# Performance work log

Measured on AMD Instinct MI355X. Metric: run time of the kernel, lower is better.

Reference implementation:

```python
import jax, jax.numpy as jnp
import numpy as np

N_USER, N_ITEM = 100000, 50000
D, H, B, E = 64, 64, 16384, 2000000

def _xavier(key, shape):
    fan_in, fan_out = shape[0], shape[1]
    lim = float(np.sqrt(6.0 / (fan_in + fan_out)))
    return jax.random.uniform(key, shape, jnp.float32, -lim, lim)

def setup_inputs() -> dict:
    key = jax.random.key(0)
    ks = jax.random.split(key, 16)
    inp = {
        "user_table": _xavier(ks[0], (N_USER, D)),
        "item_table": _xavier(ks[1], (N_ITEM, D)),
        "Wu": _xavier(ks[2], (D, D)),   # GCN_user weight ([in,out])
        "bu": jnp.zeros((D,), jnp.float32),
        "Wi": _xavier(ks[3], (D, D)),   # GCN_item weight
        "bi": jnp.zeros((D,), jnp.float32),
        "W1": _xavier(ks[4], (4 * D, 2 * H)),
        "b1": jnp.zeros((2 * H,), jnp.float32),
        "W2": _xavier(ks[5], (2 * H, H)),
        "b2": jnp.zeros((H,), jnp.float32),
        "W3": _xavier(ks[6], (H, 1)),
        "b3": jnp.zeros((1,), jnp.float32),
        "user_bias": jnp.zeros((N_USER, 1), jnp.float32),
        "item_bias": jnp.zeros((N_ITEM, 1), jnp.float32),
        "user_id": jax.random.randint(ks[7], (B,), 0, N_USER),
        "item_id": jax.random.randint(ks[8], (B,), 0, N_ITEM),
        "edge_user": jax.random.randint(ks[9], (E,), 0, N_USER),
        "edge_item": jax.random.randint(ks[10], (E,), 0, N_ITEM),
    }
    return inp

def reference(user_table, item_table, Wu, bu, Wi, bi, W1, b1, W2, b2, W3, b3,
              user_bias, item_bias, user_id, item_id, edge_user, edge_item):
    # sparse.mm(edge_ui, item_h)[user_id]: aggregate item embeddings per user
    agg_i = jax.ops.segment_sum(item_table[edge_item], edge_user, num_segments=N_USER)[user_id]
    agg_u = jax.ops.segment_sum(user_table[edge_user], edge_item, num_segments=N_ITEM)[item_id]
    ones_e = jnp.ones((edge_user.shape[0],), jnp.float32)
    deg_u = jax.ops.segment_sum(ones_e, edge_user, num_segments=N_USER)[user_id] + 1.0  # item_din
    deg_i = jax.ops.segment_sum(ones_e, edge_item, num_segments=N_ITEM)[item_id] + 1.0  # user_din
    gcn_item_h = agg_i / deg_u[:, None]   # [B, D]
    gcn_user_h = agg_u / deg_i[:, None]   # [B, D]
    # dropout p=0.3 is identity in eval mode
    gcn_user_out = jax.nn.relu(gcn_user_h @ Wu + bu)
    gcn_item_out = jax.nn.relu(gcn_item_h @ Wi + bi)
    u_emb = user_table[user_id]
    i_emb = item_table[item_id]
    x = jnp.concatenate([u_emb * i_emb,
                         u_emb * gcn_item_out,
                         gcn_user_out * i_emb,
                         gcn_user_out * gcn_item_out], axis=-1)  # [B, 4D]
    x1 = jnp.tanh(x @ W1 + b1)
    x2 = jnp.tanh(x1 @ W2 + b2)
    x3 = (x2 @ W3 + b3).reshape(-1)
    return x3 + user_bias[user_id, 0] + item_bias[item_id, 0]
```

## Files before the change

kernel.cpp:

```cpp
#include <hip/hip_runtime.h>
#include <cstdint>
#include <cstddef>

#define D 64
#define CAPU 96
#define CAPI 128
#define OCAP 4096
#define GR 32

__global__ __launch_bounds__(256) void k_build_maps(const int* __restrict__ user_id,
                                                    const int* __restrict__ item_id,
                                                    int* __restrict__ map_u,
                                                    int* __restrict__ map_i, int B)
{
    int i = blockIdx.x * blockDim.x + threadIdx.x;
    if (i < B) {
        atomicCAS(&map_u[user_id[i]], -1, i);
        atomicCAS(&map_i[item_id[i]], -1, i);
    }
}

__global__ __launch_bounds__(256) void k_scatter(const int* __restrict__ edge_user,
                                                 const int* __restrict__ edge_item,
                                                 const int* __restrict__ map_u,
                                                 const int* __restrict__ map_i,
                                                 int* __restrict__ cntU,
                                                 int* __restrict__ cntI,
                                                 uint32_t* __restrict__ listU,
                                                 uint32_t* __restrict__ listI,
                                                 int* __restrict__ ovfCnt,
                                                 uint32_t* __restrict__ ovf, int E)
{
    int t = blockIdx.x * blockDim.x + threadIdx.x;
    int base = t * 2;
    if (base >= E) return;

    int u0, u1 = -1, i0, i1 = 0;
    if (base + 2 <= E) {
        int2 eu = *(const int2*)(edge_user + base);
        int2 ei = *(const int2*)(edge_item + base);
        u0 = eu.x; u1 = eu.y; i0 = ei.x; i1 = ei.y;
    } else {
        u0 = edge_user[base]; i0 = edge_item[base];
    }

    int su0 = map_u[u0];
    int si0 = map_i[i0];
    int su1 = (u1 >= 0) ? map_u[u1] : -1;
    int si1 = (u1 >= 0) ? map_i[i1] : -1;

    if (su0 >= 0) {
        int pos = atomicAdd(&cntU[su0 * 16], 1);
        if (pos < CAPU) listU[(size_t)su0 * CAPU + pos] = (uint32_t)i0;
        else { int o = atomicAdd(ovfCnt, 1);
               if (o < OCAP) ovf[o] = ((uint32_t)su0 << 17) | (uint32_t)i0; }
    }
    if (si0 >= 0) {
        int pos = atomicAdd(&cntI[si0 * 16], 1);
        if (pos < CAPI) listI[(size_t)si0 * CAPI + pos] = (uint32_t)u0;
        else { int o = atomicAdd(ovfCnt, 1);
               if (o < OCAP) ovf[o] = 0x80000000u | ((uint32_t)si0 << 17) | (uint32_t)u0; }
    }
    if (su1 >= 0) {
        int pos = atomicAdd(&cntU[su1 * 16], 1);
        if (pos < CAPU) listU[(size_t)su1 * CAPU + pos] = (uint32_t)i1;
        else { int o = atomicAdd(ovfCnt, 1);
               if (o < OCAP) ovf[o] = ((uint32_t)su1 << 17) | (uint32_t)i1; }
    }
    if (si1 >= 0) {
        int pos = atomicAdd(&cntI[si1 * 16], 1);
        if (pos < CAPI) listI[(size_t)si1 * CAPI + pos] = (uint32_t)u1;
        else { int o = atomicAdd(ovfCnt, 1);
               if (o < OCAP) ovf[o] = 0x80000000u | ((uint32_t)si1 << 17) | (uint32_t)u1; }
    }
}

__global__ __launch_bounds__(256) void k_gather(const uint32_t* __restrict__ listU,
                                                const uint32_t* __restrict__ listI,
                                                const int* __restrict__ cntU,
                                                const int* __restrict__ cntI,
                                                const float* __restrict__ user_table,
                                                const float* __restrict__ item_table,
                                                const int* __restrict__ ovfCnt,
                                                const uint32_t* __restrict__ ovf,
                                                float* __restrict__ aggIU,
                                                float* __restrict__ aggUI, int B)
{
    int gg = (blockIdx.x * blockDim.x + threadIdx.x) >> 4;
    if (gg >= 2 * B) return;
    int l16 = threadIdx.x & 15;
    int side = gg >= B;
    int slot = side ? gg - B : gg;

    int cnt = side ? cntI[slot * 16] : cntU[slot * 16];
    int caps = side ? CAPI : CAPU;
    int n = cnt < caps ? cnt : caps;
    const uint32_t* list = side ? (listI + (size_t)slot * CAPI)
                                : (listU + (size_t)slot * CAPU);
    const float4* table4 = (const float4*)(side ? user_table : item_table);

    float4 a0 = {0.f,0.f,0.f,0.f}, a1 = {0.f,0.f,0.f,0.f};
    float4 a2 = {0.f,0.f,0.f,0.f}, a3 = {0.f,0.f,0.f,0.f};
    int j = 0;
    for (; j + 8 <= n; j += 8) {
        int r0 = (int)list[j],   r1 = (int)list[j+1], r2 = (int)list[j+2], r3 = (int)list[j+3];
        int r4 = (int)list[j+4], r5 = (int)list[j+5], r6 = (int)list[j+6], r7 = (int)list[j+7];
        float4 v0 = table4[(size_t)r0 * 16 + l16];
        float4 v1 = table4[(size_t)r1 * 16 + l16];
        float4 v2 = table4[(size_t)r2 * 16 + l16];
        float4 v3 = table4[(size_t)r3 * 16 + l16];
        float4 v4 = table4[(size_t)r4 * 16 + l16];
        float4 v5 = table4[(size_t)r5 * 16 + l16];
        float4 v6 = table4[(size_t)r6 * 16 + l16];
        float4 v7 = table4[(size_t)r7 * 16 + l16];
        a0.x += v0.x; a0.y += v0.y; a0.z += v0.z; a0.w += v0.w;
        a1.x += v1.x; a1.y += v1.y; a1.z += v1.z; a1.w += v1.w;
        a2.x += v2.x; a2.y += v2.y; a2.z += v2.z; a2.w += v2.w;
        a3.x += v3.x; a3.y += v3.y; a3.z += v3.z; a3.w += v3.w;
        a0.x += v4.x; a0.y += v4.y; a0.z += v4.z; a0.w += v4.w;
        a1.x += v5.x; a1.y += v5.y; a1.z += v5.z; a1.w += v5.w;
        a2.x += v6.x; a2.y += v6.y; a2.z += v6.z; a2.w += v6.w;
        a3.x += v7.x; a3.y += v7.y; a3.z += v7.z; a3.w += v7.w;
    }
    for (; j < n; ++j) {
        int r0 = (int)list[j];
        float4 v0 = table4[(size_t)r0 * 16 + l16];
        a0.x += v0.x; a0.y += v0.y; a0.z += v0.z; a0.w += v0.w;
    }
    if (cnt > caps) {
        int on = *ovfCnt; if (on > OCAP) on = OCAP;
        for (int k = 0; k < on; ++k) {
            uint32_t p = ovf[k];
            if ((int)(p >> 31) == side && (int)((p >> 17) & 0x3FFFu) == slot) {
                float4 v = table4[(size_t)(p & 0x1FFFFu) * 16 + l16];
                a0.x += v.x; a0.y += v.y; a0.z += v.z; a0.w += v.w;
            }
        }
    }
    float inv = 1.0f / ((float)cnt + 1.0f);
    float4 acc = {(a0.x+a1.x+a2.x+a3.x) * inv, (a0.y+a1.y+a2.y+a3.y) * inv,
                  (a0.z+a1.z+a2.z+a3.z) * inv, (a0.w+a1.w+a2.w+a3.w) * inv};
    float4* agg4 = (float4*)(side ? aggUI : aggIU);
    agg4[(size_t)slot * 16 + l16] = acc;
}

__global__ __launch_bounds__(256) void k_gcn_mlp(const int* __restrict__ user_id,
                                                 const int* __restrict__ item_id,
                                                 const int* __restrict__ map_u,
                                                 const int* __restrict__ map_i,
                                                 const float* __restrict__ aggIU,
                                                 const float* __restrict__ aggUI,
                                                 const float* __restrict__ user_table,
                                                 const float* __restrict__ item_table,
                                                 const float* __restrict__ Wi,
                                                 const float* __restrict__ bi,
                                                 const float* __restrict__ Wu,
                                                 const float* __restrict__ bu,
                                                 const float* __restrict__ W1,
                                                 const float* __restrict__ b1,
                                                 const float* __restrict__ W2,
                                                 const float* __restrict__ b2,
                                                 const float* __restrict__ W3,
                                                 const float* __restrict__ b3,
                                                 const float* __restrict__ user_bias,
                                                 const float* __restrict__ item_bias,
                                                 float* __restrict__ out, int B)
{
    __shared__ float XgiL[GR][68];
    __shared__ float XguL[GR][68];
    __shared__ float Fbuf[2 * GR][68];
    __shared__ float WB[8192];
    __shared__ int sU[GR], sI[GR];
    int t = threadIdx.x;
    int row0 = blockIdx.x * GR;
    if (t < GR) { sU[t] = user_id[row0 + t]; sI[t] = item_id[row0 + t]; }
    __syncthreads();

    int txg = t & 15, tyg = t >> 4;
    {
        const float4* agg4 = (const float4*)aggIU;
        #pragma unroll
        for (int q = 0; q < 2; ++q) {
            int idx = t * 2 + q; int r = idx >> 4, l16 = idx & 15;
            int slot = map_u[sU[r]];
            ((float4*)&Fbuf[r][0])[l16] = agg4[(size_t)slot * 16 + l16];
        }
        const float4* wg = (const float4*)Wi;
        float4* d = (float4*)WB;
        #pragma unroll
        for (int q = 0; q < 4; ++q) d[t + q * 256] = wg[t + q * 256];
    }
    __syncthreads();
    {
        float acc[2][4] = {};
        for (int k = 0; k < 64; ++k) {
            float a0 = Fbuf[2 * tyg][k], a1 = Fbuf[2 * tyg + 1][k];
            #pragma unroll
            for (int c = 0; c < 4; ++c) {
                float w = WB[k * 64 + txg + 16 * c];
                acc[0][c] = fmaf(a0, w, acc[0][c]);
                acc[1][c] = fmaf(a1, w, acc[1][c]);
            }
        }
        #pragma unroll
        for (int r = 0; r < 2; ++r)
            #pragma unroll
            for (int c = 0; c < 4; ++c)
                XgiL[2 * tyg + r][txg + 16 * c] = fmaxf(acc[r][c] + bi[txg + 16 * c], 0.f);
    }
    __syncthreads();
    {
        const float4* agg4 = (const float4*)aggUI;
        #pragma unroll
        for (int q = 0; q < 2; ++q) {
            int idx = t * 2 + q; int r = idx >> 4, l16 = idx & 15;
            int slot = map_i[sI[r]];
            ((float4*)&Fbuf[r][0])[l16] = agg4[(size_t)slot * 16 + l16];
        }
        const float4* wg = (const float4*)Wu;
        float4* d = (float4*)WB;
        #pragma unroll
        for (int q = 0; q < 4; ++q) d[t + q * 256] = wg[t + q * 256];
    }
    __syncthreads();
    {
        float acc[2][4] = {};
        for (int k = 0; k < 64; ++k) {
            float a0 = Fbuf[2 * tyg][k], a1 = Fbuf[2 * tyg + 1][k];
            #pragma unroll
            for (int c = 0; c < 4; ++c) {
                float w = WB[k * 64 + txg + 16 * c];
                acc[0][c] = fmaf(a0, w, acc[0][c]);
                acc[1][c] = fmaf(a1, w, acc[1][c]);
            }
        }
        #pragma unroll
        for (int r = 0; r < 2; ++r)
            #pragma unroll
            for (int c = 0; c < 4; ++c)
                XguL[2 * tyg + r][txg + 16 * c] = fmaxf(acc[r][c] + bu[txg + 16 * c], 0.f);
    }
    __syncthreads();

    #pragma unroll
    for (int q = 0; q < 2; ++q) {
        int idx = t * 2 + q; int r = idx >> 4, l16 = idx & 15;
        ((float4*)&Fbuf[r][0])[l16] = ((const float4*)user_table)[(size_t)sU[r] * 16 + l16];
        ((float4*)&Fbuf[GR + r][0])[l16] = ((const float4*)item_table)[(size_t)sI[r] * 16 + l16];
    }

    int tx1 = t & 31, ty1 = t >> 5;
    float acc1[4][4] = {};
    for (int j = 0; j < 4; ++j) {
        {
            const float4* w4 = (const float4*)W1 + (size_t)j * 2048;
            float4* d = (float4*)WB;
            #pragma unroll
            for (int q = 0; q < 8; ++q) d[t + q * 256] = w4[t + q * 256];
        }
        __syncthreads();
        const float (*FA)[68] = (j < 2) ? (const float (*)[68])&Fbuf[0] : (const float (*)[68])XguL;
        const float (*FB)[68] = ((j & 1) == 0) ? (const float (*)[68])&Fbuf[GR] : (const float (*)[68])XgiL;
        for (int k = 0; k < 64; ++k) {
            float a[4], b[4];
            #pragma unroll
            for (int r = 0; r < 4; ++r) a[r] = FA[4 * ty1 + r][k] * FB[4 * ty1 + r][k];
            #pragma unroll
            for (int c = 0; c < 4; ++c) b[c] = WB[k * 128 + tx1 + 32 * c];
            #pragma unroll
            for (int r = 0; r < 4; ++r)
                #pragma unroll
                for (int c = 0; c < 4; ++c)
                    acc1[r][c] = fmaf(a[r], b[c], acc1[r][c]);
        }
        __syncthreads();
    }

    float* x1t = &Fbuf[0][0];
    #pragma unroll
    for (int r = 0; r < 4; ++r)
        #pragma unroll
        for (int c = 0; c < 4; ++c) {
            int col = tx1 + 32 * c;
            x1t[(4 * ty1 + r) * 132 + col] = tanhf(acc1[r][c] + b1[col]);
        }
    {
        const float4* w4 = (const float4*)W2;
        float4* d = (float4*)WB;
        #pragma unroll
        for (int q = 0; q < 8; ++q) d[t + q * 256] = w4[t + q * 256];
    }
    __syncthreads();

    int tx2 = t & 15, ty2 = t >> 4;
    float acc2[2][4] = {};
    for (int k = 0; k < 128; ++k) {
        float a0 = x1t[(2 * ty2) * 132 + k];
        float a1 = x1t[(2 * ty2 + 1) * 132 + k];
        #pragma unroll
        for (int c = 0; c < 4; ++c) {
            float w = WB[k * 64 + tx2 + 16 * c];
            acc2[0][c] = fmaf(a0, w, acc2[0][c]);
            acc2[1][c] = fmaf(a1, w, acc2[1][c]);
        }
    }
    float b3v = b3[0];
    #pragma unroll
    for (int r = 0; r < 2; ++r) {
        int lr = 2 * ty2 + r;
        float p = 0.f;
        #pragma unroll
        for (int c = 0; c < 4; ++c) {
            int col = tx2 + 16 * c;
            p += tanhf(acc2[r][c] + b2[col]) * W3[col];
        }
        p += __shfl_xor(p, 1);
        p += __shfl_xor(p, 2);
        p += __shfl_xor(p, 4);
        p += __shfl_xor(p, 8);
        if (tx2 == 0)
            out[row0 + lr] = p + b3v + user_bias[sU[lr]] + item_bias[sI[lr]];
    }
}

extern "C" void kernel_launch(void* const* d_in, const int* in_sizes, int n_in,
                              void* d_out, int out_size, void* d_ws, size_t ws_size,
                              hipStream_t stream)
{
    const float* user_table = (const float*)d_in[0];
    const float* item_table = (const float*)d_in[1];
    const float* Wu = (const float*)d_in[2];
    const float* bu = (const float*)d_in[3];
    const float* Wi = (const float*)d_in[4];
    const float* bi = (const float*)d_in[5];
    const float* W1 = (const float*)d_in[6];
    const float* b1 = (const float*)d_in[7];
    const float* W2 = (const float*)d_in[8];
    const float* b2 = (const float*)d_in[9];
    const float* W3 = (const float*)d_in[10];
    const float* b3 = (const float*)d_in[11];
    const float* user_bias = (const float*)d_in[12];
    const float* item_bias = (const float*)d_in[13];
    const int* user_id = (const int*)d_in[14];
    const int* item_id = (const int*)d_in[15];
    const int* edge_user = (const int*)d_in[16];
    const int* edge_item = (const int*)d_in[17];

    const int N_USER = in_sizes[0] / D;
    const int N_ITEM = in_sizes[1] / D;
    const int B = in_sizes[14];
    const int E = in_sizes[16];

    char* ws = (char*)d_ws;
    size_t off = 0;
    const size_t aggIU_off = off; off += (size_t)B * D * 4;
    const size_t aggUI_off = off; off += (size_t)B * D * 4;
    const size_t mapu_off  = off; off += (size_t)N_USER * 4;
    const size_t mapi_off  = off; off += (size_t)N_ITEM * 4;
    const size_t cntU_off  = off; off += (size_t)B * 16 * 4;
    const size_t cntI_off  = off; off += (size_t)B * 16 * 4;
    const size_t ovfc_off  = off; off += 256;
    const size_t ovf_off   = off; off += (size_t)OCAP * 4;
    const size_t listU_off = off; off += (size_t)B * CAPU * 4;
    const size_t listI_off = off; off += (size_t)B * CAPI * 4;

    float* aggIU = (float*)(ws + aggIU_off);
    float* aggUI = (float*)(ws + aggUI_off);
    int*   map_u = (int*)(ws + mapu_off);
    int*   map_i = (int*)(ws + mapi_off);
    int*   cntU  = (int*)(ws + cntU_off);
    int*   cntI  = (int*)(ws + cntI_off);
    int*   ovfCnt = (int*)(ws + ovfc_off);
    uint32_t* ovf = (uint32_t*)(ws + ovf_off);
    uint32_t* listU = (uint32_t*)(ws + listU_off);
    uint32_t* listI = (uint32_t*)(ws + listI_off);

    hipMemsetAsync(ws + mapu_off, 0xFF, (size_t)(N_USER + N_ITEM) * 4, stream);
    hipMemsetAsync(ws + cntU_off, 0, (size_t)B * 16 * 4 * 2 + 256 + OCAP * 4, stream);

    k_build_maps<<<(B + 255) / 256, 256, 0, stream>>>(user_id, item_id, map_u, map_i, B);

    k_scatter<<<(E / 2 + 255) / 256, 256, 0, stream>>>(edge_user, edge_item, map_u, map_i,
                                                       cntU, cntI, listU, listI, ovfCnt, ovf, E);

    k_gather<<<(2 * B) / 16, 256, 0, stream>>>(listU, listI, cntU, cntI,
                                               user_table, item_table, ovfCnt, ovf,
                                               aggIU, aggUI, B);

    k_gcn_mlp<<<B / GR, 256, 0, stream>>>(user_id, item_id, map_u, map_i,
                                          aggIU, aggUI, user_table, item_table,
                                          Wi, bi, Wu, bu, W1, b1, W2, b2, W3, b3,
                                          user_bias, item_bias, (float*)d_out, B);
}
```

Before: 232.0 us.

## Use 512 threads in GCN/MLP kernel and merge the two GCN transforms

The final fused GCN+MLP kernel now runs with 512 threads per block instead of 256, so each thread handles fewer output rows in every GEMM stage. The two GCN projections (Wi and Wu) are loaded into shared memory together and computed in one pass, which removes a load/sync phase. Slot lookups from the maps are hoisted into shared memory once per block. The risk is that the larger blocks and smaller per-thread tiles give less register reuse and may lower occupancy, and only the last of the four kernels is affected.

Result: slower. 244.0 us (+5.2%).

```diff
diff --git a/kernel.cpp b/kernel.cpp
--- a/kernel.cpp
+++ b/kernel.cpp
@@ -144,7 +144,7 @@
     agg4[(size_t)slot * 16 + l16] = acc;
 }
 
-__global__ __launch_bounds__(256) void k_gcn_mlp(const int* __restrict__ user_id,
+__global__ __launch_bounds__(512) void k_gcn_mlp(const int* __restrict__ user_id,
                                                  const int* __restrict__ item_id,
                                                  const int* __restrict__ map_u,
                                                  const int* __restrict__ map_i,
@@ -170,105 +170,75 @@
     __shared__ float XguL[GR][68];
     __shared__ float Fbuf[2 * GR][68];
     __shared__ float WB[8192];
-    __shared__ int sU[GR], sI[GR];
+    __shared__ int sU[GR], sI[GR], slU[GR], slI[GR];
     int t = threadIdx.x;
     int row0 = blockIdx.x * GR;
-    if (t < GR) { sU[t] = user_id[row0 + t]; sI[t] = item_id[row0 + t]; }
+    if (t < GR) {
+        int u = user_id[row0 + t], it = item_id[row0 + t];
+        sU[t] = u; sI[t] = it;
+        slU[t] = map_u[u]; slI[t] = map_i[it];
+    }
     __syncthreads();
 
-    int txg = t & 15, tyg = t >> 4;
     {
-        const float4* agg4 = (const float4*)aggIU;
-        #pragma unroll
-        for (int q = 0; q < 2; ++q) {
-            int idx = t * 2 + q; int r = idx >> 4, l16 = idx & 15;
-            int slot = map_u[sU[r]];
-            ((float4*)&Fbuf[r][0])[l16] = agg4[(size_t)slot * 16 + l16];
-        }
-        const float4* wg = (const float4*)Wi;
+        int r = t >> 4, l16 = t & 15;
+        ((float4*)&Fbuf[r][0])[l16]      = ((const float4*)aggIU)[(size_t)slU[r] * 16 + l16];
+        ((float4*)&Fbuf[GR + r][0])[l16] = ((const float4*)aggUI)[(size_t)slI[r] * 16 + l16];
+        const float4* wi4 = (const float4*)Wi;
+        const float4* wu4 = (const float4*)Wu;
         float4* d = (float4*)WB;
-        #pragma unroll
-        for (int q = 0; q < 4; ++q) d[t + q * 256] = wg[t + q * 256];
+        d[t] = wi4[t];       d[t + 512] = wi4[t + 512];
+        d[1024 + t] = wu4[t]; d[1024 + t + 512] = wu4[t + 512];
     }
     __syncthreads();
+
+    int tx = t & 15, ty = t >> 4;
     {
-        float acc[2][4] = {};
+        float acci[4] = {}, accu[4] = {};
         for (int k = 0; k < 64; ++k) {
-            float a0 = Fbuf[2 * tyg][k], a1 = Fbuf[2 * tyg + 1][k];
+            float ai = Fbuf[ty][k];
+            float au = Fbuf[GR + ty][k];
             #pragma unroll
             for (int c = 0; c < 4; ++c) {
-                float w = WB[k * 64 + txg + 16 * c];
-                acc[0][c] = fmaf(a0, w, acc[0][c]);
-                acc[1][c] = fmaf(a1, w, acc[1][c]);
+                acci[c] = fmaf(ai, WB[k * 64 + tx + 16 * c], acci[c]);
+                accu[c] = fmaf(au, WB[4096 + k * 64 + tx + 16 * c], accu[c]);
             }
         }
         #pragma unroll
-        for (int r = 0; r < 2; ++r)
-            #pragma unroll
-            for (int c = 0; c < 4; ++c)
-                XgiL[2 * tyg + r][txg + 16 * c] = fmaxf(acc[r][c] + bi[txg + 16 * c], 0.f);
+        for (int c = 0; c < 4; ++c) {
+            int col = tx + 16 * c;
+            XgiL[ty][col] = fmaxf(acci[c] + bi[col], 0.f);
+            XguL[ty][col] = fmaxf(accu[c] + bu[col], 0.f);
+        }
     }
     __syncthreads();
+
     {
-        const float4* agg4 = (const float4*)aggUI;
-        #pragma unroll
-        for (int q = 0; q < 2; ++q) {
-            int idx = t * 2 + q; int r = idx >> 4, l16 = idx & 15;
-            int slot = map_i[sI[r]];
-            ((float4*)&Fbuf[r][0])[l16] = agg4[(size_t)slot * 16 + l16];
-        }
-        const float4* wg = (const float4*)Wu;
-        float4* d = (float4*)WB;
-        #pragma unroll
-        for (int q = 0; q < 4; ++q) d[t + q * 256] = wg[t + q * 256];
-    }
-    __syncthreads();
-    {
-        float acc[2][4] = {};
-        for (int k = 0; k < 64; ++k) {
-            float a0 = Fbuf[2 * tyg][k], a1 = Fbuf[2 * tyg + 1][k];
-            #pragma unroll
-            for (int c = 0; c < 4; ++c) {
-                float w = WB[k * 64 + txg + 16 * c];
-                acc[0][c] = fmaf(a0, w, acc[0][c]);
-                acc[1][c] = fmaf(a1, w, acc[1][c]);
-            }
-        }
-        #pragma unroll
-        for (int r = 0; r < 2; ++r)
-            #pragma unroll
-            for (int c = 0; c < 4; ++c)
-                XguL[2 * tyg + r][txg + 16 * c] = fmaxf(acc[r][c] + bu[txg + 16 * c], 0.f);
-    }
-    __syncthreads();
-
-    #pragma unroll
-    for (int q = 0; q < 2; ++q) {
-        int idx = t * 2 + q; int r = idx >> 4, l16 = idx & 15;
-        ((float4*)&Fbuf[r][0])[l16] = ((const float4*)user_table)[(size_t)sU[r] * 16 + l16];
+        int r = t >> 4, l16 = t & 15;
+        ((float4*)&Fbuf[r][0])[l16]      = ((const float4*)user_table)[(size_t)sU[r] * 16 + l16];
         ((float4*)&Fbuf[GR + r][0])[l16] = ((const float4*)item_table)[(size_t)sI[r] * 16 + l16];
     }
 
     int tx1 = t & 31, ty1 = t >> 5;
-    float acc1[4][4] = {};
+    float acc1[2][4] = {};
     for (int j = 0; j < 4; ++j) {
         {
             const float4* w4 = (const float4*)W1 + (size_t)j * 2048;
             float4* d = (float4*)WB;
             #pragma unroll
-            for (int q = 0; q < 8; ++q) d[t + q * 256] = w4[t + q * 256];
+            for (int q = 0; q < 4; ++q) d[t + q * 512] = w4[t + q * 512];
         }
         __syncthreads();
         const float (*FA)[68] = (j < 2) ? (const float (*)[68])&Fbuf[0] : (const float (*)[68])XguL;
         const float (*FB)[68] = ((j & 1) == 0) ? (const float (*)[68])&Fbuf[GR] : (const float (*)[68])XgiL;
         for (int k = 0; k < 64; ++k) {
-            float a[4], b[4];
-            #pragma unroll
-            for (int r = 0; r < 4; ++r) a[r] = FA[4 * ty1 + r][k] * FB[4 * ty1 + r][k];
+            float a[2], b[4];
+            a[0] = FA[2 * ty1][k]     * FB[2 * ty1][k];
+            a[1] = FA[2 * ty1 + 1][k] * FB[2 * ty1 + 1][k];
             #pragma unroll
             for (int c = 0; c < 4; ++c) b[c] = WB[k * 128 + tx1 + 32 * c];
             #pragma unroll
-            for (int r = 0; r < 4; ++r)
+            for (int r = 0; r < 2; ++r)
                 #pragma unroll
                 for (int c = 0; c < 4; ++c)
                     acc1[r][c] = fmaf(a[r], b[c], acc1[r][c]);
@@ -278,49 +248,39 @@
 
     float* x1t = &Fbuf[0][0];
     #pragma unroll
-    for (int r = 0; r < 4; ++r)
+    for (int r = 0; r < 2; ++r)
         #pragma unroll
         for (int c = 0; c < 4; ++c) {
             int col = tx1 + 32 * c;
-            x1t[(4 * ty1 + r) * 132 + col] = tanhf(acc1[r][c] + b1[col]);
+            x1t[(2 * ty1 + r) * 132 + col] = tanhf(acc1[r][c] + b1[col]);
         }
     {
         const float4* w4 = (const float4*)W2;
         float4* d = (float4*)WB;
         #pragma unroll
-        for (int q = 0; q < 8; ++q) d[t + q * 256] = w4[t + q * 256];
+        for (int q = 0; q < 4; ++q) d[t + q * 512] = w4[t + q * 512];
     }
     __syncthreads();
 
-    int tx2 = t & 15, ty2 = t >> 4;
-    float acc2[2][4] = {};
+    float acc2[4] = {};
     for (int k = 0; k < 128; ++k) {
-        float a0 = x1t[(2 * ty2) * 132 + k];
-        float a1 = x1t[(2 * ty2 + 1) * 132 + k];
+        float a0 = x1t[ty * 132 + k];
         #pragma unroll
-        for (int c = 0; c < 4; ++c) {
-            float w = WB[k * 64 + tx2 + 16 * c];
-            acc2[0][c] = fmaf(a0, w, acc2[0][c]);
-            acc2[1][c] = fmaf(a1, w, acc2[1][c]);
-        }
-    }
-    float b3v = b3[0];
+        for (int c = 0; c < 4; ++c)
+            acc2[c] = fmaf(a0, WB[k * 64 + tx + 16 * c], acc2[c]);
+    }
+    float p = 0.f;
     #pragma unroll
-    for (int r = 0; r < 2; ++r) {
-        int lr = 2 * ty2 + r;
-        float p = 0.f;
-        #pragma unroll
-        for (int c = 0; c < 4; ++c) {
-            int col = tx2 + 16 * c;
-            p += tanhf(acc2[r][c] + b2[col]) * W3[col];
-        }
-        p += __shfl_xor(p, 1);
-        p += __shfl_xor(p, 2);
-        p += __shfl_xor(p, 4);
-        p += __shfl_xor(p, 8);
-        if (tx2 == 0)
-            out[row0 + lr] = p + b3v + user_bias[sU[lr]] + item_bias[sI[lr]];
-    }
+    for (int c = 0; c < 4; ++c) {
+        int col = tx + 16 * c;
+        p += tanhf(acc2[c] + b2[col]) * W3[col];
+    }
+    p += __shfl_xor(p, 1);
+    p += __shfl_xor(p, 2);
+    p += __shfl_xor(p, 4);
+    p += __shfl_xor(p, 8);
+    if (tx == 0)
+        out[row0 + ty] = p + b3[0] + user_bias[sU[ty]] + item_bias[sI[ty]];
 }
 
 extern "C" void kernel_launch(void* const* d_in, const int* in_sizes, int n_in,
@@ -387,7 +347,7 @@
                                                user_table, item_table, ovfCnt, ovf,
                                                aggIU, aggUI, B);
 
-    k_gcn_mlp<<<B / GR, 256, 0, stream>>>(user_id, item_id, map_u, map_i,
+    k_gcn_mlp<<<B / GR, 512, 0, stream>>>(user_id, item_id, map_u, map_i,
                                           aggIU, aggUI, user_table, item_table,
                                           Wi, bi, Wu, bu, W1, b1, W2, b2, W3, b3,
                                           user_bias, item_bias, (float*)d_out, B);
```
